# Kernel tuning notes

Hardware: AMD Instinct MI355X
Metric: run time of the kernel (lower is better)

Reference implementation:

```python
import jax, jax.numpy as jnp
import numpy as np

B, T, C, H = 8, 2048, 1024, 16
S = C // H
LN_EPS = 1e-5


def setup_inputs() -> dict:
    key = jax.random.key(0)
    ks = jax.random.split(key, 12)
    w = lambda k: jax.random.normal(k, (C, C), dtype=jnp.float32) * 0.02
    return {
        "x": jax.random.normal(ks[0], (B, T, C), dtype=jnp.float32),
        "time_mix_k": jax.random.uniform(ks[1], (1, 1, C), dtype=jnp.float32),
        "time_mix_v": jax.random.uniform(ks[2], (1, 1, C), dtype=jnp.float32),
        "time_mix_r": jax.random.uniform(ks[3], (1, 1, C), dtype=jnp.float32),
        # keep exp(time_decay) < 1 for numerical stability over T=2048 steps
        "time_decay": -jax.random.uniform(ks[4], (H, S), minval=0.1, maxval=5.0, dtype=jnp.float32),
        "time_first": jax.random.uniform(ks[5], (H, S), dtype=jnp.float32),
        "Wk": w(ks[6]), "Wv": w(ks[7]), "Wr": w(ks[8]), "Wo": w(ks[9]),
        "ln_g": jnp.ones((C,), jnp.float32),
        "ln_b": jnp.zeros((C,), jnp.float32),
    }


def reference(x, time_mix_k, time_mix_v, time_mix_r, time_decay, time_first, Wk, Wv, Wr, Wo, ln_g, ln_b):
    Bx, Tx, Cx = x.shape
    # time_shift: xx[t] = x[t-1], xx[0] = 0
    xx = jnp.pad(x, ((0, 0), (1, 0), (0, 0)))[:, :-1]
    xk = x * time_mix_k + xx * (1 - time_mix_k)
    xv = x * time_mix_v + xx * (1 - time_mix_v)
    xr = x * time_mix_r + xx * (1 - time_mix_r)
    proj = lambda z, W: jnp.einsum('btc,dc->btd', z, W).reshape(Bx, Tx, H, S)
    k = proj(xk, Wk)  # [B,T,H,S]
    v = proj(xv, Wv)
    r = proj(xr, Wr)
    kv = k * v  # elementwise per-channel 'at' (diagonal of outer-product state)
    decay = jnp.exp(time_decay)  # [H,S]

    def step(state, inp):
        kv_t, r_t = inp  # [B,H,S] each
        state = kv_t + decay * state
        o = r_t * (time_first * kv_t + state)
        return state, o

    kvT = jnp.swapaxes(kv, 0, 1)  # [T,B,H,S]
    rT = jnp.swapaxes(r, 0, 1)
    _, outT = jax.lax.scan(step, jnp.zeros((Bx, H, S), x.dtype), (kvT, rT))
    out = jnp.swapaxes(outT, 0, 1).reshape(Bx, Tx, Cx)
    mu = out.mean(-1, keepdims=True)
    var = out.var(-1, keepdims=True)
    out = (out - mu) / jnp.sqrt(var + LN_EPS) * ln_g + ln_b
    return jnp.einsum('btc,dc->btd', out, Wo)
```

## Files before the change

kernel.cpp:

```cpp
#include <hip/hip_runtime.h>

#define Bsz 8
#define Tn  2048
#define Cn  1024
#define Hn  16
#define Sn  64
#define Mn  (Bsz * Tn)
#define NC  32
#define LCH (Tn / NC)
#define Kd  1024
#define NKT (Kd / 64)

typedef __attribute__((ext_vector_type(8))) short bf16x8;
typedef __attribute__((ext_vector_type(4))) float f32x4;

__device__ __forceinline__ unsigned short f2bf(float f) {
  union { float f; unsigned int u; } v;
  v.f = f;
  unsigned int r = (v.u + 0x7FFFu + ((v.u >> 16) & 1u)) >> 16;
  return (unsigned short)r;
}
__device__ __forceinline__ float bf2f(unsigned short u) {
  union { unsigned int u; float f; } v;
  v.u = ((unsigned int)u) << 16;
  return v.f;
}

__global__ void wconv_kernel(const float* __restrict__ Wk, const float* __restrict__ Wv,
                             const float* __restrict__ Wr, const float* __restrict__ Wo,
                             unsigned short* __restrict__ out) {
  int i = blockIdx.x * blockDim.x + threadIdx.x;
  int which = i >> 18;
  int off = (i & 0x3FFFF) * 4;
  const float* src = which == 0 ? Wk : which == 1 ? Wv : which == 2 ? Wr : Wo;
  float4 f = *(const float4*)(src + off);
  ushort4 o;
  o.x = f2bf(f.x); o.y = f2bf(f.y); o.z = f2bf(f.z); o.w = f2bf(f.w);
  *(ushort4*)(out + (size_t)which * (Cn * Cn) + off) = o;
}

__global__ void mix3_kernel(const float* __restrict__ x,
                            const float* __restrict__ tmk, const float* __restrict__ tmv,
                            const float* __restrict__ tmr,
                            unsigned short* __restrict__ ok, unsigned short* __restrict__ ov,
                            unsigned short* __restrict__ orr) {
  int idx = blockIdx.x * blockDim.x + threadIdx.x;
  int c4 = idx & (Cn / 4 - 1);
  int bt = idx >> 8;
  int t = bt & (Tn - 1);
  size_t base = (size_t)bt * Cn + c4 * 4;
  float4 xv = *(const float4*)(x + base);
  float4 xxv = {0.f, 0.f, 0.f, 0.f};
  if (t != 0) xxv = *(const float4*)(x + base - Cn);
  float4 dx = {xv.x - xxv.x, xv.y - xxv.y, xv.z - xxv.z, xv.w - xxv.w};
  float4 tk = *(const float4*)(tmk + c4 * 4);
  float4 tv = *(const float4*)(tmv + c4 * 4);
  float4 tr = *(const float4*)(tmr + c4 * 4);
  ushort4 a, b, c;
  a.x = f2bf(xxv.x + tk.x * dx.x); a.y = f2bf(xxv.y + tk.y * dx.y);
  a.z = f2bf(xxv.z + tk.z * dx.z); a.w = f2bf(xxv.w + tk.w * dx.w);
  b.x = f2bf(xxv.x + tv.x * dx.x); b.y = f2bf(xxv.y + tv.y * dx.y);
  b.z = f2bf(xxv.z + tv.z * dx.z); b.w = f2bf(xxv.w + tv.w * dx.w);
  c.x = f2bf(xxv.x + tr.x * dx.x); c.y = f2bf(xxv.y + tr.y * dx.y);
  c.z = f2bf(xxv.z + tr.z * dx.z); c.w = f2bf(xxv.w + tr.w * dx.w);
  *(ushort4*)(ok + base) = a;
  *(ushort4*)(ov + base) = b;
  *(ushort4*)(orr + base) = c;
}

__device__ __forceinline__ void gload_lds16(const void* g, void* l) {
  __builtin_amdgcn_global_load_lds((const __attribute__((address_space(1))) void*)g,
                                   (__attribute__((address_space(3))) void*)l, 16, 0, 0);
}

template <bool OUTBF16>
__global__ __launch_bounds__(512, 2) void gemm256(const unsigned short* __restrict__ A,
                                                  const unsigned short* __restrict__ Bt,
                                                  void* __restrict__ Cm) {
  __shared__ unsigned short lds[65536];
  char* ldsc = (char*)lds;
  const int tid = threadIdx.x;
  const int wid = tid >> 6, lane = tid & 63;
  const int wm = wid >> 2, wn = wid & 3;
  int bid = ((int)blockIdx.x & 7) * 32 + ((int)blockIdx.x >> 3);
  const int mt = bid >> 2, nt = bid & 3;
  const int m0 = mt * 256, n0 = nt * 256;

  const unsigned short* Ag = A + (size_t)m0 * Kd;
  const unsigned short* Bg = Bt + (size_t)n0 * Kd;

  auto stage = [&](const unsigned short* gbase, int gcol0, int ldsoff) {
#pragma unroll
    for (int j = 0; j < 2; ++j) {
      int c = tid + j * 512;
      int row = c >> 2, cc = c & 3;
      const unsigned short* g = gbase + (size_t)row * Kd + gcol0 + ((cc ^ ((row >> 1) & 3)) << 3);
      gload_lds16(g, ldsc + ldsoff + (wid * 64 + j * 512) * 16);
    }
  };

  const int l15 = lane & 15, lg = lane >> 4;
  const int axr = (lg ^ ((l15 >> 1) & 3)) << 4;
  const int arow = (wm * 128 + l15) * 64;
  const int brow = (wn * 64 + l15) * 64;

  f32x4 acc[8][4] = {};

  stage(Ag, 0, 0);
  stage(Bg, 0, 32768);
  asm volatile("" ::: "memory");
  stage(Ag, 32, 16384);
  stage(Bg, 32, 49152);

#pragma unroll 2
  for (int kt = 0; kt < NKT; ++kt) {
    const int bbase = (kt & 1) << 16;
    const int nbase = bbase ^ 65536;
    const int k1 = (kt + 1) * 64;
    const bool st = (kt < NKT - 1);

    if (st) { stage(Ag, k1, nbase); stage(Bg, k1, nbase + 32768); }
    if (st) asm volatile("s_waitcnt vmcnt(8)" ::: "memory");
    else    asm volatile("s_waitcnt vmcnt(4)" ::: "memory");
    __builtin_amdgcn_s_barrier();
    __builtin_amdgcn_sched_barrier(0);
    {
      bf16x8 bfr[4], afr[8];
#pragma unroll
      for (int nj = 0; nj < 4; ++nj)
        bfr[nj] = *(const bf16x8*)(ldsc + bbase + 32768 + brow + nj * 1024 + axr);
#pragma unroll
      for (int mi = 0; mi < 8; ++mi)
        afr[mi] = *(const bf16x8*)(ldsc + bbase + arow + mi * 1024 + axr);
      __builtin_amdgcn_s_setprio(1);
#pragma unroll
      for (int mi = 0; mi < 8; ++mi)
#pragma unroll
        for (int nj = 0; nj < 4; ++nj)
          acc[mi][nj] = __builtin_amdgcn_mfma_f32_16x16x32_bf16(afr[mi], bfr[nj], acc[mi][nj], 0, 0, 0);
      __builtin_amdgcn_s_setprio(0);
    }

    if (st) { stage(Ag, k1 + 32, nbase + 16384); stage(Bg, k1 + 32, nbase + 49152); }
    if (st) asm volatile("s_waitcnt vmcnt(8)" ::: "memory");
    else    asm volatile("s_waitcnt vmcnt(0)" ::: "memory");
    __builtin_amdgcn_s_barrier();
    __builtin_amdgcn_sched_barrier(0);
    {
      bf16x8 bfr[4], afr[8];
#pragma unroll
      for (int nj = 0; nj < 4; ++nj)
        bfr[nj] = *(const bf16x8*)(ldsc + bbase + 49152 + brow + nj * 1024 + axr);
#pragma unroll
      for (int mi = 0; mi < 8; ++mi)
        afr[mi] = *(const bf16x8*)(ldsc + bbase + 16384 + arow + mi * 1024 + axr);
      __builtin_amdgcn_s_setprio(1);
#pragma unroll
      for (int mi = 0; mi < 8; ++mi)
#pragma unroll
        for (int nj = 0; nj < 4; ++nj)
          acc[mi][nj] = __builtin_amdgcn_mfma_f32_16x16x32_bf16(afr[mi], bfr[nj], acc[mi][nj], 0, 0, 0);
      __builtin_amdgcn_s_setprio(0);
    }
  }

#pragma unroll
  for (int mi = 0; mi < 8; ++mi)
#pragma unroll
    for (int nj = 0; nj < 4; ++nj)
#pragma unroll
      for (int rr = 0; rr < 4; ++rr) {
        int row = m0 + wm * 128 + mi * 16 + (lane >> 4) * 4 + rr;
        int col = n0 + wn * 64 + nj * 16 + (lane & 15);
        if (OUTBF16)
          ((unsigned short*)Cm)[(size_t)row * Cn + col] = f2bf(acc[mi][nj][rr]);
        else
          ((float*)Cm)[(size_t)row * Cn + col] = acc[mi][nj][rr];
      }
}

__global__ void scan_phase1(const unsigned short* __restrict__ k,
                            const unsigned short* __restrict__ v,
                            const float* __restrict__ td, float* __restrict__ cs) {
  int blk = blockIdx.x;
  int c = blk & (NC - 1);
  int bh = blk >> 5;
  int b = bh >> 4;
  int h = bh & 15;
  int s = threadIdx.x;
  float decay = expf(td[h * Sn + s]);
  size_t base = ((size_t)(b * Tn + c * LCH)) * Cn + h * Sn + s;
  float st = 0.f;
#pragma unroll 8
  for (int i = 0; i < LCH; ++i) {
    float kv = bf2f(k[base]) * bf2f(v[base]);
    st = kv + decay * st;
    base += Cn;
  }
  cs[(size_t)blk * Sn + s] = st;
}

__global__ void scan_phase2(const float* __restrict__ td, float* __restrict__ cs) {
  int bh = blockIdx.x;
  int h = bh & 15;
  int s = threadIdx.x;
  float dL = expf(td[h * Sn + s] * (float)LCH);
  float carry = 0.f;
  for (int c = 0; c < NC; ++c) {
    size_t idx = ((size_t)bh * NC + c) * Sn + s;
    float sc = cs[idx];
    cs[idx] = carry;
    carry = sc + dL * carry;
  }
}

__global__ void scan_phase3(const unsigned short* __restrict__ k,
                            const unsigned short* __restrict__ v,
                            const unsigned short* __restrict__ r,
                            const float* __restrict__ td, const float* __restrict__ tf,
                            const float* __restrict__ cs,
                            unsigned short* __restrict__ out) {
  int blk = blockIdx.x;
  int c = blk & (NC - 1);
  int bh = blk >> 5;
  int b = bh >> 4;
  int h = bh & 15;
  int s = threadIdx.x;
  float decay = expf(td[h * Sn + s]);
  float first = tf[h * Sn + s];
  float st = cs[(size_t)blk * Sn + s];
  size_t base = ((size_t)(b * Tn + c * LCH)) * Cn + h * Sn + s;
#pragma unroll 8
  for (int i = 0; i < LCH; ++i) {
    float kv = bf2f(k[base]) * bf2f(v[base]);
    st = kv + decay * st;
    out[base] = f2bf(bf2f(r[base]) * (first * kv + st));
    base += Cn;
  }
}

__global__ __launch_bounds__(256) void ln_kernel(const unsigned short* __restrict__ in,
                                                 const float* __restrict__ g,
                                                 const float* __restrict__ bb,
                                                 unsigned short* __restrict__ out) {
  int row = blockIdx.x;
  int tid = threadIdx.x;
  size_t base = (size_t)row * Cn + tid * 4;
  ushort4 uv = *(const ushort4*)(in + base);
  float4 xv = {bf2f(uv.x), bf2f(uv.y), bf2f(uv.z), bf2f(uv.w)};
  float sum = xv.x + xv.y + xv.z + xv.w;
  float ss = xv.x * xv.x + xv.y * xv.y + xv.z * xv.z + xv.w * xv.w;
#pragma unroll
  for (int off = 32; off >= 1; off >>= 1) {
    sum += __shfl_down(sum, off, 64);
    ss += __shfl_down(ss, off, 64);
  }
  __shared__ float s1[4], s2[4];
  if ((tid & 63) == 0) { s1[tid >> 6] = sum; s2[tid >> 6] = ss; }
  __syncthreads();
  sum = s1[0] + s1[1] + s1[2] + s1[3];
  ss = s2[0] + s2[1] + s2[2] + s2[3];
  float mu = sum * (1.f / Cn);
  float var = ss * (1.f / Cn) - mu * mu;
  float rstd = rsqrtf(var + 1e-5f);
  float4 gv = *(const float4*)(g + tid * 4);
  float4 bv = *(const float4*)(bb + tid * 4);
  ushort4 o;
  o.x = f2bf((xv.x - mu) * rstd * gv.x + bv.x);
  o.y = f2bf((xv.y - mu) * rstd * gv.y + bv.y);
  o.z = f2bf((xv.z - mu) * rstd * gv.z + bv.z);
  o.w = f2bf((xv.w - mu) * rstd * gv.w + bv.w);
  *(ushort4*)(out + base) = o;
}

extern "C" void kernel_launch(void* const* d_in, const int* in_sizes, int n_in,
                              void* d_out, int out_size, void* d_ws, size_t ws_size,
                              hipStream_t stream) {
  const float* x   = (const float*)d_in[0];
  const float* tmk = (const float*)d_in[1];
  const float* tmv = (const float*)d_in[2];
  const float* tmr = (const float*)d_in[3];
  const float* td  = (const float*)d_in[4];
  const float* tf  = (const float*)d_in[5];
  const float* Wk  = (const float*)d_in[6];
  const float* Wv  = (const float*)d_in[7];
  const float* Wr  = (const float*)d_in[8];
  const float* Wo  = (const float*)d_in[9];
  const float* lng = (const float*)d_in[10];
  const float* lnb = (const float*)d_in[11];
  float* out = (float*)d_out;

  char* ws = (char*)d_ws;
  const size_t MB = 1024 * 1024;
  unsigned short* wbf  = (unsigned short*)(ws);
  unsigned short* xk   = (unsigned short*)(ws + 8 * MB);
  unsigned short* xv_  = (unsigned short*)(ws + 40 * MB);
  unsigned short* xr   = (unsigned short*)(ws + 72 * MB);
  unsigned short* bufK = (unsigned short*)(ws + 104 * MB);
  unsigned short* bufV = (unsigned short*)(ws + 136 * MB);
  unsigned short* bufR = (unsigned short*)(ws + 168 * MB);
  unsigned short* preLN = xk;
  unsigned short* lnout = xv_;
  float* chunkS = (float*)(ws + 200 * MB);

  const int gemm_grid = (Mn / 256) * (Cn / 256);
  const int mix_grid = Mn * (Cn / 4) / 256;

  wconv_kernel<<<4 * Cn * Cn / 4 / 256, 256, 0, stream>>>(Wk, Wv, Wr, Wo, wbf);
  mix3_kernel<<<mix_grid, 256, 0, stream>>>(x, tmk, tmv, tmr, xk, xv_, xr);

  gemm256<true><<<gemm_grid, 512, 0, stream>>>(xk,  wbf + 0 * (size_t)Cn * Cn, bufK);
  gemm256<true><<<gemm_grid, 512, 0, stream>>>(xv_, wbf + 1 * (size_t)Cn * Cn, bufV);
  gemm256<true><<<gemm_grid, 512, 0, stream>>>(xr,  wbf + 2 * (size_t)Cn * Cn, bufR);

  scan_phase1<<<Bsz * Hn * NC, 64, 0, stream>>>(bufK, bufV, td, chunkS);
  scan_phase2<<<Bsz * Hn, 64, 0, stream>>>(td, chunkS);
  scan_phase3<<<Bsz * Hn * NC, 64, 0, stream>>>(bufK, bufV, bufR, td, tf, chunkS, preLN);

  ln_kernel<<<Mn, 256, 0, stream>>>(preLN, lng, lnb, lnout);

  gemm256<false><<<gemm_grid, 512, 0, stream>>>(lnout, wbf + 3 * (size_t)Cn * Cn, out);

  (void)in_sizes; (void)n_in; (void)out_size; (void)ws_size;
}
```

Before: 247.7 us.

## Switch GEMM to 32x32x16 MFMA with software-pipelined LDS fragment reads

Replaces the 16x16x32 bf16 MFMA tiling in the shared GEMM with 32x32x16 instructions, each warp computing a 4x2 grid of 32x32 accumulators. The fragment reads from LDS are double-buffered across four k-subslices so that reads for the next subslice overlap the MFMAs of the current one. The second half-tile stage is moved to the middle of the compute, with adjusted waitcnt values. This aims to cut LDS read traffic per FLOP and improve MFMA issue density, at the cost of more live registers and tighter correctness demands on the new swizzle and output mapping.

```diff
diff --git a/kernel.cpp b/kernel.cpp
--- a/kernel.cpp
+++ b/kernel.cpp
@@ -13,6 +13,7 @@
 
 typedef __attribute__((ext_vector_type(8))) short bf16x8;
 typedef __attribute__((ext_vector_type(4))) float f32x4;
+typedef __attribute__((ext_vector_type(16))) float f32x16;
 
 __device__ __forceinline__ unsigned short f2bf(float f) {
   union { float f; unsigned int u; } v;
@@ -73,6 +74,26 @@
                                    (__attribute__((address_space(3))) void*)l, 16, 0, 0);
 }
 
+#define RDK(kk, AV, BV)                                                              \
+  {                                                                                  \
+    const int ch = ((((kk) & 1) * 2 + lg) ^ swq) << 4;                               \
+    const int ub = bbase + ((kk) >> 1) * 16384 + ch;                                 \
+    _Pragma("unroll") for (int mi = 0; mi < 4; ++mi)                                 \
+        AV[mi] = *(const bf16x8*)(ldsc + ub + arow + mi * 2048);                     \
+    _Pragma("unroll") for (int nj = 0; nj < 2; ++nj)                                 \
+        BV[nj] = *(const bf16x8*)(ldsc + ub + brow + nj * 2048);                     \
+  }
+
+#define MFMA8(AV, BV)                                                                \
+  {                                                                                  \
+    __builtin_amdgcn_s_setprio(1);                                                   \
+    _Pragma("unroll") for (int mi = 0; mi < 4; ++mi)                                 \
+        _Pragma("unroll") for (int nj = 0; nj < 2; ++nj)                             \
+            acc[mi][nj] = __builtin_amdgcn_mfma_f32_32x32x16_bf16(AV[mi], BV[nj],    \
+                                                                  acc[mi][nj], 0, 0, 0); \
+    __builtin_amdgcn_s_setprio(0);                                                   \
+  }
+
 template <bool OUTBF16>
 __global__ __launch_bounds__(512, 2) void gemm256(const unsigned short* __restrict__ A,
                                                   const unsigned short* __restrict__ Bt,
@@ -99,16 +120,16 @@
     }
   };
 
-  const int l15 = lane & 15, lg = lane >> 4;
-  const int axr = (lg ^ ((l15 >> 1) & 3)) << 4;
-  const int arow = (wm * 128 + l15) * 64;
-  const int brow = (wn * 64 + l15) * 64;
-
-  f32x4 acc[8][4] = {};
+  const int l31 = lane & 31, lg = lane >> 5;
+  const int swq = (l31 >> 1) & 3;
+  const int arow = (wm * 128 + l31) * 64;
+  const int brow = 32768 + (wn * 64 + l31) * 64;
+
+  f32x16 acc[4][2] = {};
+  bf16x8 aA[4], bA[2], aB[4], bB[2];
 
   stage(Ag, 0, 0);
   stage(Bg, 0, 32768);
-  asm volatile("" ::: "memory");
   stage(Ag, 32, 16384);
   stage(Bg, 32, 49152);
 
@@ -120,62 +141,37 @@
     const bool st = (kt < NKT - 1);
 
     if (st) { stage(Ag, k1, nbase); stage(Bg, k1, nbase + 32768); }
-    if (st) asm volatile("s_waitcnt vmcnt(8)" ::: "memory");
-    else    asm volatile("s_waitcnt vmcnt(4)" ::: "memory");
-    __builtin_amdgcn_s_barrier();
-    __builtin_amdgcn_sched_barrier(0);
-    {
-      bf16x8 bfr[4], afr[8];
-#pragma unroll
-      for (int nj = 0; nj < 4; ++nj)
-        bfr[nj] = *(const bf16x8*)(ldsc + bbase + 32768 + brow + nj * 1024 + axr);
-#pragma unroll
-      for (int mi = 0; mi < 8; ++mi)
-        afr[mi] = *(const bf16x8*)(ldsc + bbase + arow + mi * 1024 + axr);
-      __builtin_amdgcn_s_setprio(1);
-#pragma unroll
-      for (int mi = 0; mi < 8; ++mi)
-#pragma unroll
-        for (int nj = 0; nj < 4; ++nj)
-          acc[mi][nj] = __builtin_amdgcn_mfma_f32_16x16x32_bf16(afr[mi], bfr[nj], acc[mi][nj], 0, 0, 0);
-      __builtin_amdgcn_s_setprio(0);
-    }
-
-    if (st) { stage(Ag, k1 + 32, nbase + 16384); stage(Bg, k1 + 32, nbase + 49152); }
-    if (st) asm volatile("s_waitcnt vmcnt(8)" ::: "memory");
+    if (st) asm volatile("s_waitcnt vmcnt(4)" ::: "memory");
     else    asm volatile("s_waitcnt vmcnt(0)" ::: "memory");
     __builtin_amdgcn_s_barrier();
     __builtin_amdgcn_sched_barrier(0);
-    {
-      bf16x8 bfr[4], afr[8];
-#pragma unroll
-      for (int nj = 0; nj < 4; ++nj)
-        bfr[nj] = *(const bf16x8*)(ldsc + bbase + 49152 + brow + nj * 1024 + axr);
-#pragma unroll
-      for (int mi = 0; mi < 8; ++mi)
-        afr[mi] = *(const bf16x8*)(ldsc + bbase + 16384 + arow + mi * 1024 + axr);
-      __builtin_amdgcn_s_setprio(1);
-#pragma unroll
-      for (int mi = 0; mi < 8; ++mi)
-#pragma unroll
-        for (int nj = 0; nj < 4; ++nj)
-          acc[mi][nj] = __builtin_amdgcn_mfma_f32_16x16x32_bf16(afr[mi], bfr[nj], acc[mi][nj], 0, 0, 0);
-      __builtin_amdgcn_s_setprio(0);
-    }
-  }
-
-#pragma unroll
-  for (int mi = 0; mi < 8; ++mi)
-#pragma unroll
-    for (int nj = 0; nj < 4; ++nj)
-#pragma unroll
-      for (int rr = 0; rr < 4; ++rr) {
-        int row = m0 + wm * 128 + mi * 16 + (lane >> 4) * 4 + rr;
-        int col = n0 + wn * 64 + nj * 16 + (lane & 15);
+
+    RDK(0, aA, bA)
+    RDK(1, aB, bB)
+    __builtin_amdgcn_sched_barrier(0);
+    MFMA8(aA, bA)
+    RDK(2, aA, bA)
+    __builtin_amdgcn_sched_barrier(0);
+    MFMA8(aB, bB)
+    if (st) { stage(Ag, k1 + 32, nbase + 16384); stage(Bg, k1 + 32, nbase + 49152); }
+    RDK(3, aB, bB)
+    __builtin_amdgcn_sched_barrier(0);
+    MFMA8(aA, bA)
+    MFMA8(aB, bB)
+  }
+
+#pragma unroll
+  for (int mi = 0; mi < 4; ++mi)
+#pragma unroll
+    for (int nj = 0; nj < 2; ++nj)
+#pragma unroll
+      for (int r = 0; r < 16; ++r) {
+        int row = m0 + wm * 128 + mi * 32 + (r & 3) + 8 * (r >> 2) + 4 * lg;
+        int col = n0 + wn * 64 + nj * 32 + l31;
         if (OUTBF16)
-          ((unsigned short*)Cm)[(size_t)row * Cn + col] = f2bf(acc[mi][nj][rr]);
+          ((unsigned short*)Cm)[(size_t)row * Cn + col] = f2bf(acc[mi][nj][r]);
         else
-          ((float*)Cm)[(size_t)row * Cn + col] = acc[mi][nj][rr];
+          ((float*)Cm)[(size_t)row * Cn + col] = acc[mi][nj][r];
       }
 }
 
```

Result: slower. 255.2 us (+3.0%).

## Rewrite GEMM as eight-phase pipelined loop with LDS-staged bf16 epilogue

Applied to the files above, without the earlier changes.

Replaces the two-half-step GEMM main loop with four sub-phases per K tile. Each phase loads a half of the A fragments plus B fragments from LDS, issues one quarter-tile global-to-LDS prefetch up to two tiles ahead, then runs 16 MFMAs between barriers. The LDS swizzle changes to a row&3 XOR pattern. The bf16 output path now transposes through LDS so it can write 16-byte coalesced stores instead of scattered 2-byte ones. The goal is finer overlap of loads with MFMA and cheaper output writes, at the cost of more barriers per tile.

```diff
diff --git a/kernel.cpp b/kernel.cpp
--- a/kernel.cpp
+++ b/kernel.cpp
@@ -73,15 +73,44 @@
                                    (__attribute__((address_space(3))) void*)l, 16, 0, 0);
 }
 
+#define PHASE(H, KS, LOADB, STAGE_STMT, VM_STMT)                                   \
+  {                                                                                \
+    _Pragma("unroll") for (int mi4 = 0; mi4 < 4; ++mi4) {                          \
+      const int row = wm * 128 + (H) * 64 + mi4 * 16 + l15;                        \
+      aF[mi4] = *(const bf16x8*)(ldsc + dbase + (KS) * 16384 + row * 64 +          \
+                                 ((lg ^ (row & 3)) << 4));                         \
+    }                                                                              \
+    if (LOADB) {                                                                   \
+      _Pragma("unroll") for (int nj = 0; nj < 4; ++nj) {                           \
+        const int row = wn * 64 + nj * 16 + l15;                                   \
+        bF[nj] = *(const bf16x8*)(ldsc + dbase + 32768 + (KS) * 16384 + row * 64 + \
+                                  ((lg ^ (row & 3)) << 4));                        \
+      }                                                                            \
+    }                                                                              \
+    STAGE_STMT;                                                                    \
+    VM_STMT;                                                                       \
+    __builtin_amdgcn_s_barrier();                                                  \
+    asm volatile("s_waitcnt lgkmcnt(0)" ::: "memory");                             \
+    __builtin_amdgcn_sched_barrier(0);                                             \
+    __builtin_amdgcn_s_setprio(1);                                                 \
+    _Pragma("unroll") for (int mi4 = 0; mi4 < 4; ++mi4)                            \
+      _Pragma("unroll") for (int nj = 0; nj < 4; ++nj)                             \
+        acc[(H) * 4 + mi4][nj] = __builtin_amdgcn_mfma_f32_16x16x32_bf16(          \
+            aF[mi4], bF[nj], acc[(H) * 4 + mi4][nj], 0, 0, 0);                     \
+    __builtin_amdgcn_s_setprio(0);                                                 \
+    __builtin_amdgcn_s_barrier();                                                  \
+  }
+
 template <bool OUTBF16>
-__global__ __launch_bounds__(512, 2) void gemm256(const unsigned short* __restrict__ A,
-                                                  const unsigned short* __restrict__ Bt,
-                                                  void* __restrict__ Cm) {
+__global__ __launch_bounds__(512, 2) void gemm8p(const unsigned short* __restrict__ A,
+                                                 const unsigned short* __restrict__ Bt,
+                                                 void* __restrict__ Cm) {
   __shared__ unsigned short lds[65536];
   char* ldsc = (char*)lds;
   const int tid = threadIdx.x;
   const int wid = tid >> 6, lane = tid & 63;
   const int wm = wid >> 2, wn = wid & 3;
+  const int l15 = lane & 15, lg = lane >> 4;
   int bid = ((int)blockIdx.x & 7) * 32 + ((int)blockIdx.x >> 3);
   const int mt = bid >> 2, nt = bid & 3;
   const int m0 = mt * 256, n0 = nt * 256;
@@ -89,94 +118,78 @@
   const unsigned short* Ag = A + (size_t)m0 * Kd;
   const unsigned short* Bg = Bt + (size_t)n0 * Kd;
 
-  auto stage = [&](const unsigned short* gbase, int gcol0, int ldsoff) {
+  auto stageR = [&](const unsigned short* gbase, int ktt, int ks, int Loff) {
 #pragma unroll
     for (int j = 0; j < 2; ++j) {
-      int c = tid + j * 512;
-      int row = c >> 2, cc = c & 3;
-      const unsigned short* g = gbase + (size_t)row * Kd + gcol0 + ((cc ^ ((row >> 1) & 3)) << 3);
-      gload_lds16(g, ldsc + ldsoff + (wid * 64 + j * 512) * 16);
+      const int row = (tid >> 2) + j * 128;
+      const int sl = tid & 3;
+      const unsigned short* g =
+          gbase + (size_t)row * Kd + ktt * 64 + ks * 32 + ((sl ^ (row & 3)) << 3);
+      gload_lds16(g, ldsc + Loff + wid * 1024 + j * 8192);
     }
   };
 
-  const int l15 = lane & 15, lg = lane >> 4;
-  const int axr = (lg ^ ((l15 >> 1) & 3)) << 4;
-  const int arow = (wm * 128 + l15) * 64;
-  const int brow = (wn * 64 + l15) * 64;
-
   f32x4 acc[8][4] = {};
-
-  stage(Ag, 0, 0);
-  stage(Bg, 0, 32768);
-  asm volatile("" ::: "memory");
-  stage(Ag, 32, 16384);
-  stage(Bg, 32, 49152);
-
-#pragma unroll 2
+  bf16x8 aF[4], bF[4];
+
+  stageR(Ag, 0, 0, 0);
+  stageR(Bg, 0, 0, 32768);
+  stageR(Ag, 0, 1, 16384);
+  stageR(Bg, 0, 1, 49152);
+  stageR(Ag, 1, 0, 65536);
+  stageR(Bg, 1, 0, 65536 + 32768);
+  asm volatile("s_waitcnt vmcnt(4)" ::: "memory");
+  __builtin_amdgcn_s_barrier();
+
   for (int kt = 0; kt < NKT; ++kt) {
-    const int bbase = (kt & 1) << 16;
-    const int nbase = bbase ^ 65536;
-    const int k1 = (kt + 1) * 64;
-    const bool st = (kt < NKT - 1);
-
-    if (st) { stage(Ag, k1, nbase); stage(Bg, k1, nbase + 32768); }
-    if (st) asm volatile("s_waitcnt vmcnt(8)" ::: "memory");
-    else    asm volatile("s_waitcnt vmcnt(4)" ::: "memory");
-    __builtin_amdgcn_s_barrier();
+    const int dbase = (kt & 1) << 16;
+    const int nd = dbase ^ 65536;
+    const bool s1 = (kt + 1 < NKT), s2 = (kt + 2 < NKT);
+    const int vmn = (kt < NKT - 2) ? 4 : 0;
+    PHASE(0, 0, 1, if (s1) stageR(Ag, kt + 1, 1, nd + 16384), ;)
+    PHASE(1, 0, 0, if (s1) stageR(Bg, kt + 1, 1, nd + 49152), ;)
+    PHASE(1, 1, 1, if (s2) stageR(Ag, kt + 2, 0, dbase), ;)
+    PHASE(0, 1, 0, if (s2) stageR(Bg, kt + 2, 0, dbase + 32768),
+          if (vmn == 4) asm volatile("s_waitcnt vmcnt(4)" ::: "memory");
+          else asm volatile("s_waitcnt vmcnt(0)" ::: "memory"))
+  }
+
+  if (OUTBF16) {
+    char* tb = ldsc + wid * 16384;
+#pragma unroll
+    for (int mi = 0; mi < 8; ++mi)
+#pragma unroll
+      for (int nj = 0; nj < 4; ++nj)
+#pragma unroll
+        for (int rr = 0; rr < 4; ++rr) {
+          const int row = mi * 16 + lg * 4 + rr;
+          const int col = nj * 16 + l15;
+          *(unsigned short*)(tb + row * 128 + ((col * 2) ^ ((row & 7) << 4))) =
+              f2bf(acc[mi][nj][rr]);
+        }
+    asm volatile("s_waitcnt lgkmcnt(0)" ::: "memory");
     __builtin_amdgcn_sched_barrier(0);
-    {
-      bf16x8 bfr[4], afr[8];
+    const int orl = lane >> 3, och = lane & 7;
+#pragma unroll
+    for (int it = 0; it < 16; ++it) {
+      const int row = it * 8 + orl;
+      uint4 vv = *(const uint4*)(tb + row * 128 + ((och * 16) ^ ((row & 7) << 4)));
+      const int gr = m0 + wm * 128 + row;
+      const int gc = n0 + wn * 64 + och * 8;
+      *(uint4*)((unsigned short*)Cm + (size_t)gr * Cn + gc) = vv;
+    }
+  } else {
+#pragma unroll
+    for (int mi = 0; mi < 8; ++mi)
 #pragma unroll
       for (int nj = 0; nj < 4; ++nj)
-        bfr[nj] = *(const bf16x8*)(ldsc + bbase + 32768 + brow + nj * 1024 + axr);
-#pragma unroll
-      for (int mi = 0; mi < 8; ++mi)
-        afr[mi] = *(const bf16x8*)(ldsc + bbase + arow + mi * 1024 + axr);
-      __builtin_amdgcn_s_setprio(1);
-#pragma unroll
-      for (int mi = 0; mi < 8; ++mi)
-#pragma unroll
-        for (int nj = 0; nj < 4; ++nj)
-          acc[mi][nj] = __builtin_amdgcn_mfma_f32_16x16x32_bf16(afr[mi], bfr[nj], acc[mi][nj], 0, 0, 0);
-      __builtin_amdgcn_s_setprio(0);
-    }
-
-    if (st) { stage(Ag, k1 + 32, nbase + 16384); stage(Bg, k1 + 32, nbase + 49152); }
-    if (st) asm volatile("s_waitcnt vmcnt(8)" ::: "memory");
-    else    asm volatile("s_waitcnt vmcnt(0)" ::: "memory");
-    __builtin_amdgcn_s_barrier();
-    __builtin_amdgcn_sched_barrier(0);
-    {
-      bf16x8 bfr[4], afr[8];
-#pragma unroll
-      for (int nj = 0; nj < 4; ++nj)
-        bfr[nj] = *(const bf16x8*)(ldsc + bbase + 49152 + brow + nj * 1024 + axr);
-#pragma unroll
-      for (int mi = 0; mi < 8; ++mi)
-        afr[mi] = *(const bf16x8*)(ldsc + bbase + 16384 + arow + mi * 1024 + axr);
-      __builtin_amdgcn_s_setprio(1);
-#pragma unroll
-      for (int mi = 0; mi < 8; ++mi)
-#pragma unroll
-        for (int nj = 0; nj < 4; ++nj)
-          acc[mi][nj] = __builtin_amdgcn_mfma_f32_16x16x32_bf16(afr[mi], bfr[nj], acc[mi][nj], 0, 0, 0);
-      __builtin_amdgcn_s_setprio(0);
-    }
-  }
-
-#pragma unroll
-  for (int mi = 0; mi < 8; ++mi)
-#pragma unroll
-    for (int nj = 0; nj < 4; ++nj)
-#pragma unroll
-      for (int rr = 0; rr < 4; ++rr) {
-        int row = m0 + wm * 128 + mi * 16 + (lane >> 4) * 4 + rr;
-        int col = n0 + wn * 64 + nj * 16 + (lane & 15);
-        if (OUTBF16)
-          ((unsigned short*)Cm)[(size_t)row * Cn + col] = f2bf(acc[mi][nj][rr]);
-        else
+#pragma unroll
+        for (int rr = 0; rr < 4; ++rr) {
+          const int row = m0 + wm * 128 + mi * 16 + lg * 4 + rr;
+          const int col = n0 + wn * 64 + nj * 16 + l15;
           ((float*)Cm)[(size_t)row * Cn + col] = acc[mi][nj][rr];
-      }
+        }
+  }
 }
 
 __global__ void scan_phase1(const unsigned short* __restrict__ k,
@@ -309,9 +322,9 @@
   wconv_kernel<<<4 * Cn * Cn / 4 / 256, 256, 0, stream>>>(Wk, Wv, Wr, Wo, wbf);
   mix3_kernel<<<mix_grid, 256, 0, stream>>>(x, tmk, tmv, tmr, xk, xv_, xr);
 
-  gemm256<true><<<gemm_grid, 512, 0, stream>>>(xk,  wbf + 0 * (size_t)Cn * Cn, bufK);
-  gemm256<true><<<gemm_grid, 512, 0, stream>>>(xv_, wbf + 1 * (size_t)Cn * Cn, bufV);
-  gemm256<true><<<gemm_grid, 512, 0, stream>>>(xr,  wbf + 2 * (size_t)Cn * Cn, bufR);
+  gemm8p<true><<<gemm_grid, 512, 0, stream>>>(xk,  wbf + 0 * (size_t)Cn * Cn, bufK);
+  gemm8p<true><<<gemm_grid, 512, 0, stream>>>(xv_, wbf + 1 * (size_t)Cn * Cn, bufV);
+  gemm8p<true><<<gemm_grid, 512, 0, stream>>>(xr,  wbf + 2 * (size_t)Cn * Cn, bufR);
 
   scan_phase1<<<Bsz * Hn * NC, 64, 0, stream>>>(bufK, bufV, td, chunkS);
   scan_phase2<<<Bsz * Hn, 64, 0, stream>>>(td, chunkS);
@@ -319,7 +332,7 @@
 
   ln_kernel<<<Mn, 256, 0, stream>>>(preLN, lng, lnb, lnout);
 
-  gemm256<false><<<gemm_grid, 512, 0, stream>>>(lnout, wbf + 3 * (size_t)Cn * Cn, out);
+  gemm8p<false><<<gemm_grid, 512, 0, stream>>>(lnout, wbf + 3 * (size_t)Cn * Cn, out);
 
   (void)in_sizes; (void)n_in; (void)out_size; (void)ws_size;
 }
```

After: 257.6 us. 4.0% more time.
